# Optimization experiments

Measured on AMD Instinct MI355X. Metric: run time of the kernel, lower is better.

The kernel has to match this reference:

```python
import jax, jax.numpy as jnp
import numpy as np

N = 8192          # total interactions in flattened batch
D = 128           # embedding_dim
H1, H2 = 512, 256 # hidden_dims
EPS_NORM = 1e-16


def _l2_normalize(x, eps=EPS_NORM):
    # matches torch.nn.functional.normalize(p=2): x / max(||x||, eps)
    n = jnp.linalg.norm(x, axis=-1, keepdims=True)
    return x / jnp.maximum(n, eps)


def setup_inputs() -> dict:
    key = jax.random.key(0)
    ks = jax.random.split(key, 10)
    ad_embeddings = jax.random.normal(ks[0], (N, D), dtype=jnp.float32)
    user = jax.random.randint(ks[1], (N,), 0, 512, dtype=jnp.int64)
    timestamp = jax.random.randint(ks[2], (N,), 0, 1000000, dtype=jnp.int64)
    is_click = jax.random.randint(ks[3], (N,), 0, 2).astype(jnp.bool_)
    # MLP params: Linear(D,H1) -> SiLU -> Linear(H1,H2) -> SiLU -> Linear(H2,D) -> L2Norm
    def lin(k, fan_in, fan_out):
        kw, kb = jax.random.split(k)
        bound = 1.0 / np.sqrt(fan_in)
        W = jax.random.uniform(kw, (fan_in, fan_out), minval=-bound, maxval=bound, dtype=jnp.float32)
        b = jax.random.uniform(kb, (fan_out,), minval=-bound, maxval=bound, dtype=jnp.float32)
        return W, b
    W1, b1 = lin(ks[4], D, H1)
    W2, b2 = lin(ks[5], H1, H2)
    W3, b3 = lin(ks[6], H2, D)
    return {"ad_embeddings": ad_embeddings, "user": user, "timestamp": timestamp,
            "is_click": is_click, "W1": W1, "b1": b1, "W2": W2, "b2": b2,
            "W3": W3, "b3": b3}


def reference(ad_embeddings, user, timestamp, is_click, W1, b1, W2, b2, W3, b3):
    dtype = ad_embeddings.dtype
    # mask[i,j] = is_click[j] & (user[i]==user[j]) & (timestamp[i] > timestamp[j])
    user_matches = user[:, None] == user[None, :]                # [N,N]
    causal = timestamp[:, None] > timestamp[None, :]             # [N,N]
    mask = (is_click[None, :] & user_matches & causal).astype(dtype)
    norm_mask = mask / (jnp.sum(mask, axis=1, keepdims=True) + 1e-16)
    history_emb = jnp.einsum('ij,jk->ik', norm_mask, ad_embeddings)  # [N,D]
    h = jax.nn.silu(history_emb @ W1 + b1)
    h = jax.nn.silu(h @ W2 + b2)
    h = h @ W3 + b3
    x = _l2_normalize(_l2_normalize(h))  # mlp's trailing L2Norm, then self.norm
    empty = jnp.linalg.norm(history_emb, axis=1, keepdims=True) == 0
    return jnp.where(empty, jnp.zeros_like(x), x)
```

## Files before the change

kernel.cpp:

```cpp
#include <hip/hip_runtime.h>
#include <hip/hip_bf16.h>
#include <math.h>


#define N_ROWS  8192
#define D_EMB   128
#define N_USERS 512
#define BUCKET  64
#define CNT_BASE ((int)0xAAAAAAAAu)

typedef __bf16 bf16;
typedef __bf16 bf16x8 __attribute__((ext_vector_type(8)));
typedef float  floatx4 __attribute__((ext_vector_type(4)));

__device__ __forceinline__ floatx4 mfma16(bf16x8 a, bf16x8 b, floatx4 c) {
    return __builtin_amdgcn_mfma_f32_16x16x32_bf16(a, b, c, 0, 0, 0);
}


__global__ __launch_bounds__(256) void k_prep(
    const int* __restrict__ user, const int* __restrict__ ts,
    const int* __restrict__ clk,
    const float* __restrict__ W1, const float* __restrict__ W2,
    const float* __restrict__ W3,
    bf16* __restrict__ Wp1, bf16* __restrict__ Wp2, bf16* __restrict__ Wp3,
    int* __restrict__ g_cnt, int2* __restrict__ g_bucket)
{
    int g = blockIdx.x * 256 + threadIdx.x;
    if (g < N_ROWS) {
        if (clk[g]) {
            int u = user[g];
            int slot = atomicAdd(&g_cnt[u], 1) - CNT_BASE;
            if (slot < BUCKET)
                g_bucket[u * BUCKET + slot] = make_int2(ts[g], g);
        }
        return;
    }
    int gc = g - N_ROWS;
    const float* W; bf16* Wp; int K, N, chunk;
    if (gc < 8192)       { W = W1; Wp = Wp1; K = 128; N = 512; chunk = gc; }
    else if (gc < 24576) { W = W2; Wp = Wp2; K = 512; N = 256; chunk = gc - 8192; }
    else                 { W = W3; Wp = Wp3; K = 256; N = 128; chunk = gc - 24576; }
    int lane = chunk & 63, blk = chunk >> 6;
    int chunks_k = K >> 5;
    int f = blk / chunks_k, k0c = blk - f * chunks_k;
    int q = lane >> 4, c = lane & 15;
    const float* src = W + (size_t)(k0c * 32 + q * 8) * N + f * 16 + c;
    bf16x8 v;
    #pragma unroll
    for (int j = 0; j < 8; ++j) v[j] = (bf16)src[(size_t)j * N];
    *(bf16x8*)&Wp[(size_t)chunk * 8] = v;
}


__global__ __launch_bounds__(512) void k_fused(
    const int* __restrict__ user, const int* __restrict__ ts,
    const float* __restrict__ ad,
    const int* __restrict__ g_cnt, const int2* __restrict__ g_bucket,
    const bf16* __restrict__ Wp1, const bf16* __restrict__ Wp2,
    const bf16* __restrict__ Wp3,
    const float* __restrict__ b1, const float* __restrict__ b2,
    const float* __restrict__ b3,
    float* __restrict__ out)
{
    __shared__ __align__(16) char smem[59008];
    bf16 (*Ah)[136] = (bf16(*)[136])smem;
    bf16 (*H1)[520] = (bf16(*)[520])(smem + 8704);
    bf16 (*H2)[264] = (bf16(*)[264])(smem + 8704 + 33280);
    float (*O)[132] = (float(*)[132])smem;
    int* s_empty    = (int*)(smem + 58880);

    const int t = threadIdx.x;
    const int w = t >> 6, lane = t & 63;
    const int q = lane >> 4, c = lane & 15;
    const int m0 = blockIdx.x * 32;

    bf16x8 pb1[4][4];
    #pragma unroll
    for (int cf = 0; cf < 4; ++cf)
        #pragma unroll
        for (int k0c = 0; k0c < 4; ++k0c)
            pb1[cf][k0c] = *(const bf16x8*)&Wp1[(size_t)(((w * 4 + cf) * 4 + k0c) * 64 + lane) * 8];
    bf16x8 pb3[8];
    #pragma unroll
    for (int k0c = 0; k0c < 8; ++k0c)
        pb3[k0c] = *(const bf16x8*)&Wp3[(size_t)((w * 8 + k0c) * 64 + lane) * 8];
    bf16x8 pb2a[2][8];
    #pragma unroll
    for (int cf = 0; cf < 2; ++cf)
        #pragma unroll
        for (int k0c = 0; k0c < 8; ++k0c)
            pb2a[cf][k0c] = *(const bf16x8*)&Wp2[(size_t)(((w * 2 + cf) * 16 + k0c) * 64 + lane) * 8];

    {
        const int row = t >> 4, dl = t & 15;
        const int i = m0 + row;
        const int u = user[i], myts = ts[i];
        int cnt = g_cnt[u] - CNT_BASE;
        cnt = (cnt > BUCKET) ? BUCKET : cnt;
        const int beg = u * BUCKET, end = beg + cnt;
        float a[8] = {0.f, 0.f, 0.f, 0.f, 0.f, 0.f, 0.f, 0.f};
        int m = 0;
        const float* adp = ad + (size_t)dl * 8;
        for (int p = beg; p < end; p += 4) {
            #pragma unroll
            for (int kk = 0; kk < 4; ++kk) {
                int pp = p + kk;
                int ppc = (pp < end) ? pp : end - 1;
                int2 it = g_bucket[ppc];
                bool ok = (pp < end) & (it.x < myts);
                const float4* r = (const float4*)(adp + (size_t)it.y * D_EMB);
                float4 v0 = r[0], v1 = r[1];
                float s = ok ? 1.f : 0.f;
                a[0] += s * v0.x; a[1] += s * v0.y; a[2] += s * v0.z; a[3] += s * v0.w;
                a[4] += s * v1.x; a[5] += s * v1.y; a[6] += s * v1.z; a[7] += s * v1.w;
                m += ok ? 1 : 0;
            }
        }
        float inv = m ? 1.f / (float)m : 0.f;
        bf16x8 hv;
        #pragma unroll
        for (int j = 0; j < 8; ++j) hv[j] = (bf16)(a[j] * inv);
        *(bf16x8*)&Ah[row][dl * 8] = hv;
        if (dl == 0) s_empty[row] = (m == 0);
    }
    __syncthreads();

    {
        floatx4 acc[4][2];
        #pragma unroll
        for (int cf = 0; cf < 4; ++cf)
            #pragma unroll
            for (int mi = 0; mi < 2; ++mi)
                acc[cf][mi] = (floatx4){0.f, 0.f, 0.f, 0.f};
        #pragma unroll
        for (int k0c = 0; k0c < 4; ++k0c) {
            bf16x8 a0 = *(const bf16x8*)&Ah[c][k0c * 32 + q * 8];
            bf16x8 a1 = *(const bf16x8*)&Ah[16 + c][k0c * 32 + q * 8];
            #pragma unroll
            for (int cf = 0; cf < 4; ++cf) {
                acc[cf][0] = mfma16(a0, pb1[cf][k0c], acc[cf][0]);
                acc[cf][1] = mfma16(a1, pb1[cf][k0c], acc[cf][1]);
            }
        }
        #pragma unroll
        for (int cf = 0; cf < 4; ++cf) {
            const int col = w * 64 + cf * 16 + c;
            const float bb = b1[col];
            #pragma unroll
            for (int mi = 0; mi < 2; ++mi)
                #pragma unroll
                for (int r = 0; r < 4; ++r) {
                    float v = acc[cf][mi][r] + bb;
                    v = v / (1.f + __expf(-v));
                    H1[mi * 16 + q * 4 + r][col] = (bf16)v;
                }
        }
    }
    __syncthreads();

    {
        floatx4 acc[2][2];
        #pragma unroll
        for (int cf = 0; cf < 2; ++cf)
            #pragma unroll
            for (int mi = 0; mi < 2; ++mi)
                acc[cf][mi] = (floatx4){0.f, 0.f, 0.f, 0.f};
        #pragma unroll
        for (int k0c = 0; k0c < 16; ++k0c) {
            bf16x8 a0 = *(const bf16x8*)&H1[c][k0c * 32 + q * 8];
            bf16x8 a1 = *(const bf16x8*)&H1[16 + c][k0c * 32 + q * 8];
            #pragma unroll
            for (int cf = 0; cf < 2; ++cf) {
                bf16x8 b = (k0c < 8)
                    ? pb2a[cf][k0c & 7]
                    : *(const bf16x8*)&Wp2[(size_t)(((w * 2 + cf) * 16 + k0c) * 64 + lane) * 8];
                acc[cf][0] = mfma16(a0, b, acc[cf][0]);
                acc[cf][1] = mfma16(a1, b, acc[cf][1]);
            }
        }
        #pragma unroll
        for (int cf = 0; cf < 2; ++cf) {
            const int col = w * 32 + cf * 16 + c;
            const float bb = b2[col];
            #pragma unroll
            for (int mi = 0; mi < 2; ++mi)
                #pragma unroll
                for (int r = 0; r < 4; ++r) {
                    float v = acc[cf][mi][r] + bb;
                    v = v / (1.f + __expf(-v));
                    H2[mi * 16 + q * 4 + r][col] = (bf16)v;
                }
        }
    }
    __syncthreads();

    {
        floatx4 acc0 = (floatx4){0.f, 0.f, 0.f, 0.f};
        floatx4 acc1 = (floatx4){0.f, 0.f, 0.f, 0.f};
        #pragma unroll
        for (int k0c = 0; k0c < 8; ++k0c) {
            bf16x8 a0 = *(const bf16x8*)&H2[c][k0c * 32 + q * 8];
            bf16x8 a1 = *(const bf16x8*)&H2[16 + c][k0c * 32 + q * 8];
            acc0 = mfma16(a0, pb3[k0c], acc0);
            acc1 = mfma16(a1, pb3[k0c], acc1);
        }
        const int col = w * 16 + c;
        const float bb = b3[col];
        #pragma unroll
        for (int r = 0; r < 4; ++r) {
            O[q * 4 + r][col]      = acc0[r] + bb;
            O[16 + q * 4 + r][col] = acc1[r] + bb;
        }
    }
    __syncthreads();

    {
        const int row = t >> 4, s = t & 15;
        float v[8];
        const float* orow = &O[row][s * 8];
        float ss = 0.f;
        #pragma unroll
        for (int j = 0; j < 8; ++j) { v[j] = orow[j]; ss += v[j] * v[j]; }
        ss += __shfl_xor(ss, 1);
        ss += __shfl_xor(ss, 2);
        ss += __shfl_xor(ss, 4);
        ss += __shfl_xor(ss, 8);
        float scale = s_empty[row] ? 0.f : 1.f / fmaxf(sqrtf(ss), 1e-16f);
        float4 o0 = {v[0] * scale, v[1] * scale, v[2] * scale, v[3] * scale};
        float4 o1 = {v[4] * scale, v[5] * scale, v[6] * scale, v[7] * scale};
        float* dst = out + (size_t)(m0 + row) * D_EMB + s * 8;
        *(float4*)dst       = o0;
        *(float4*)(dst + 4) = o1;
    }
}


extern "C" void kernel_launch(void* const* d_in, const int* in_sizes, int n_in,
                              void* d_out, int out_size, void* d_ws, size_t ws_size,
                              hipStream_t stream) {
    const float* ad   = (const float*)d_in[0];
    const int*   user = (const int*)d_in[1];
    const int*   ts   = (const int*)d_in[2];
    const int*   clk  = (const int*)d_in[3];
    const float* W1 = (const float*)d_in[4];
    const float* b1 = (const float*)d_in[5];
    const float* W2 = (const float*)d_in[6];
    const float* b2 = (const float*)d_in[7];
    const float* W3 = (const float*)d_in[8];
    const float* b3 = (const float*)d_in[9];
    float* out = (float*)d_out;
    (void)in_sizes; (void)n_in; (void)out_size; (void)ws_size;

    char* ws = (char*)d_ws;
    bf16* Wp1      = (bf16*)(ws);
    bf16* Wp2      = (bf16*)(ws + 131072);
    bf16* Wp3      = (bf16*)(ws + 393216);
    int*  g_cnt    = (int*) (ws + 458752);
    int2* g_bucket = (int2*)(ws + 460800);

    k_prep <<<dim3(144), dim3(256), 0, stream>>>(user, ts, clk, W1, W2, W3,
                                                 Wp1, Wp2, Wp3, g_cnt, g_bucket);
    k_fused<<<dim3(N_ROWS / 32), dim3(512), 0, stream>>>(user, ts, ad,
                                                         g_cnt, g_bucket,
                                                         Wp1, Wp2, Wp3,
                                                         b1, b2, b3, out);
}
```

Baseline: 91.60 us.

## Stage per-user bucket entries in LDS and defer W2/W3 register loads

Each row's 64 bucket entries (timestamp, index) are now copied from global memory into shared memory with vector loads at kernel start. The gather loop then runs a fixed 64-slot trip and uses a negative index as the empty-slot sentinel, so the per-user count load and the dependent global bucket reads go away. The W2/W3 fragment loads are moved behind a sched_barrier until after the gather, which lowers register pressure during the gather. In exchange the loop always covers 64 slots, issuing dummy loads of row 0 for empty slots. It also relies on unused bucket slots holding a negative index, which depends on how the workspace was initialised.

Result: slower. 95.57 us (+4.3%).

```diff
diff --git a/kernel.cpp b/kernel.cpp
--- a/kernel.cpp
+++ b/kernel.cpp
@@ -56,7 +56,7 @@
 __global__ __launch_bounds__(512) void k_fused(
     const int* __restrict__ user, const int* __restrict__ ts,
     const float* __restrict__ ad,
-    const int* __restrict__ g_cnt, const int2* __restrict__ g_bucket,
+    const int2* __restrict__ g_bucket,
     const bf16* __restrict__ Wp1, const bf16* __restrict__ Wp2,
     const bf16* __restrict__ Wp3,
     const float* __restrict__ b1, const float* __restrict__ b2,
@@ -68,12 +68,23 @@
     bf16 (*H1)[520] = (bf16(*)[520])(smem + 8704);
     bf16 (*H2)[264] = (bf16(*)[264])(smem + 8704 + 33280);
     float (*O)[132] = (float(*)[132])smem;
+    int2 (*s_bucket)[BUCKET] = (int2(*)[BUCKET])(smem + 8704 + 33280);
     int* s_empty    = (int*)(smem + 58880);
 
     const int t = threadIdx.x;
     const int w = t >> 6, lane = t & 63;
     const int q = lane >> 4, c = lane & 15;
     const int m0 = blockIdx.x * 32;
+    const int row = t >> 4, dl = t & 15;
+
+    const int i_row = m0 + row;
+    const int u = user[i_row], myts = ts[i_row];
+    {
+        const int4* gb = (const int4*)&g_bucket[u * BUCKET + dl * 4];
+        int4 e0 = gb[0], e1 = gb[1];
+        *(int4*)&s_bucket[row][dl * 4]     = e0;
+        *(int4*)&s_bucket[row][dl * 4 + 2] = e1;
+    }
 
     bf16x8 pb1[4][4];
     #pragma unroll
@@ -81,35 +92,22 @@
         #pragma unroll
         for (int k0c = 0; k0c < 4; ++k0c)
             pb1[cf][k0c] = *(const bf16x8*)&Wp1[(size_t)(((w * 4 + cf) * 4 + k0c) * 64 + lane) * 8];
-    bf16x8 pb3[8];
-    #pragma unroll
-    for (int k0c = 0; k0c < 8; ++k0c)
-        pb3[k0c] = *(const bf16x8*)&Wp3[(size_t)((w * 8 + k0c) * 64 + lane) * 8];
-    bf16x8 pb2a[2][8];
-    #pragma unroll
-    for (int cf = 0; cf < 2; ++cf)
-        #pragma unroll
-        for (int k0c = 0; k0c < 8; ++k0c)
-            pb2a[cf][k0c] = *(const bf16x8*)&Wp2[(size_t)(((w * 2 + cf) * 16 + k0c) * 64 + lane) * 8];
-
-    {
-        const int row = t >> 4, dl = t & 15;
-        const int i = m0 + row;
-        const int u = user[i], myts = ts[i];
-        int cnt = g_cnt[u] - CNT_BASE;
-        cnt = (cnt > BUCKET) ? BUCKET : cnt;
-        const int beg = u * BUCKET, end = beg + cnt;
+
+    {
         float a[8] = {0.f, 0.f, 0.f, 0.f, 0.f, 0.f, 0.f, 0.f};
         int m = 0;
         const float* adp = ad + (size_t)dl * 8;
-        for (int p = beg; p < end; p += 4) {
+        #pragma unroll 2
+        for (int p = 0; p < BUCKET; p += 4) {
+            int4 e0 = *(const int4*)&s_bucket[row][p];
+            int4 e1 = *(const int4*)&s_bucket[row][p + 2];
+            int xs[4] = {e0.x, e0.z, e1.x, e1.z};
+            int ys[4] = {e0.y, e0.w, e1.y, e1.w};
             #pragma unroll
             for (int kk = 0; kk < 4; ++kk) {
-                int pp = p + kk;
-                int ppc = (pp < end) ? pp : end - 1;
-                int2 it = g_bucket[ppc];
-                bool ok = (pp < end) & (it.x < myts);
-                const float4* r = (const float4*)(adp + (size_t)it.y * D_EMB);
+                bool ok = (ys[kk] >= 0) & (xs[kk] < myts);
+                int idx = ok ? ys[kk] : 0;
+                const float4* r = (const float4*)(adp + (size_t)idx * D_EMB);
                 float4 v0 = r[0], v1 = r[1];
                 float s = ok ? 1.f : 0.f;
                 a[0] += s * v0.x; a[1] += s * v0.y; a[2] += s * v0.z; a[3] += s * v0.w;
@@ -124,6 +122,18 @@
         *(bf16x8*)&Ah[row][dl * 8] = hv;
         if (dl == 0) s_empty[row] = (m == 0);
     }
+
+    __builtin_amdgcn_sched_barrier(0);
+    bf16x8 pb3[8];
+    #pragma unroll
+    for (int k0c = 0; k0c < 8; ++k0c)
+        pb3[k0c] = *(const bf16x8*)&Wp3[(size_t)((w * 8 + k0c) * 64 + lane) * 8];
+    bf16x8 pb2a[2][8];
+    #pragma unroll
+    for (int cf = 0; cf < 2; ++cf)
+        #pragma unroll
+        for (int k0c = 0; k0c < 8; ++k0c)
+            pb2a[cf][k0c] = *(const bf16x8*)&Wp2[(size_t)(((w * 2 + cf) * 16 + k0c) * 64 + lane) * 8];
     __syncthreads();
 
     {
@@ -216,9 +226,8 @@
     __syncthreads();
 
     {
-        const int row = t >> 4, s = t & 15;
         float v[8];
-        const float* orow = &O[row][s * 8];
+        const float* orow = &O[row][dl * 8];
         float ss = 0.f;
         #pragma unroll
         for (int j = 0; j < 8; ++j) { v[j] = orow[j]; ss += v[j] * v[j]; }
@@ -229,7 +238,7 @@
         float scale = s_empty[row] ? 0.f : 1.f / fmaxf(sqrtf(ss), 1e-16f);
         float4 o0 = {v[0] * scale, v[1] * scale, v[2] * scale, v[3] * scale};
         float4 o1 = {v[4] * scale, v[5] * scale, v[6] * scale, v[7] * scale};
-        float* dst = out + (size_t)(m0 + row) * D_EMB + s * 8;
+        float* dst = out + (size_t)(m0 + row) * D_EMB + dl * 8;
         *(float4*)dst       = o0;
         *(float4*)(dst + 4) = o1;
     }
@@ -262,7 +271,7 @@
     k_prep <<<dim3(144), dim3(256), 0, stream>>>(user, ts, clk, W1, W2, W3,
                                                  Wp1, Wp2, Wp3, g_cnt, g_bucket);
     k_fused<<<dim3(N_ROWS / 32), dim3(512), 0, stream>>>(user, ts, ad,
-                                                         g_cnt, g_bucket,
+                                                         g_bucket,
                                                          Wp1, Wp2, Wp3,
                                                          b1, b2, b3, out);
 }
```
